# Kernel optimization log

Measured on AMD Instinct MI355X. Metric: run time of the kernel, lower is better.

Reference implementation:

```python
import jax, jax.numpy as jnp
import numpy as np

EULER = 0.5772156649015329  # Euler-Mascheroni constant


def _expi_neg(t):
    """Ei(t) for t < 0, via Ei(t) = -E1(-t).

    E1 uses the power series for x < 8 and the asymptotic expansion for x >= 8.
    This replaces the scipy.special.expi CPU round-trip of the original module.
    """
    x = -t  # x > 0
    # --- series branch (x < 8): E1(x) = -gamma - ln(x) + sum_{k>=1} (-1)^{k+1} x^k/(k*k!)
    xs = jnp.minimum(x, 8.0)
    s = jnp.zeros_like(xs)
    term = xs  # (-1)^{k+1} xs^k / k!  starting at k=1
    for k in range(1, 31):
        s = s + term / k
        term = term * (-xs) / (k + 1)
    e1_small = -EULER - jnp.log(xs) + s
    # --- asymptotic branch (x >= 8): E1(x) ~ e^{-x}/x * sum_n (-1)^n n! / x^n
    xl = jnp.maximum(x, 8.0)
    a = jnp.ones_like(xl)
    acc = jnp.ones_like(xl)
    for n in range(1, 9):
        a = a * (-n) / xl
        acc = acc + a
    e1_large = jnp.exp(-xl) / xl * acc
    e1 = jnp.where(x < 8.0, e1_small, e1_large)
    return -e1


def _li(v):
    # logarithmic integral li(v) = Ei(ln v); constant w.r.t. params (scipy detaches in torch)
    return jax.lax.stop_gradient(_expi_neg(jnp.log(v)))


def _phi(u, var2, var3, var4, var5):
    log_term = jnp.log(1.0 - u)
    li_term = _li(1.0 - u)
    return (var2 / log_term
            + var3 * li_term
            + var4 * ((1.0 - u) / log_term - li_term)
            + var5 * ((1.0 - u) * (log_term + 1.0) / (2.0 * log_term ** 2) - li_term / 2.0))


def setup_inputs() -> dict:
    key = jax.random.key(0)
    B, L, D = 262144, 64, 32
    hidden = [128, 128, 64]
    ks = jax.random.split(key, 16)
    u = jax.random.uniform(ks[0], (B, L), dtype=jnp.float32, minval=1e-4, maxval=1.0 - 1e-4)
    dims = [L] + hidden + [D]
    inp = {"u": u}
    for i in range(4):
        inp[f"W{i}"] = jax.random.normal(ks[1 + 2 * i], (dims[i], dims[i + 1]), dtype=jnp.float32) / np.sqrt(dims[i]).astype(np.float32)
        inp[f"b{i}"] = jnp.zeros((dims[i + 1],), dtype=jnp.float32)
    for j in range(1, 7):
        inp[f"var{j}"] = jax.random.normal(ks[8 + j], (1, D), dtype=jnp.float32) * 0.1
    return inp


def reference(u, W0, b0, W1, b1, W2, b2, W3, b3, var1, var2, var3, var4, var5, var6):
    # MLP: three Linear+ReLU blocks then final Linear to dim_data
    h = u
    for W, b in ((W0, b0), (W1, b1), (W2, b2)):
        h = jax.nn.relu(h @ W + b)
    net = h @ W3 + b3  # (B, dim_data)
    D = net.shape[1]
    ud = u[:, :D]
    # spline corrections
    p01 = -4.0 * ud ** 5 + 5.0 * ud ** 4
    corr1 = jnp.nan_to_num(p01 * (var1 + _phi(ud, var2, var3, var4, var5)), nan=0.0)
    corr2 = var6 * (ud ** 3 - 2.0 * ud ** 2 + ud)
    net_tif = jax.nn.relu(net + corr1 + corr2)
    # inverse TIF activation: ((1 - u^2)/2)^{-x}
    return jnp.power((1.0 - ud ** 2) / 2.0, -net_tif)
```

## Files before the change

kernel.cpp:

```cpp
#include <hip/hip_runtime.h>
#include <hip/hip_bf16.h>
#include <math.h>

#define LN2_F 0.69314718055994531f

typedef _Float16 half8 __attribute__((ext_vector_type(8)));
typedef _Float16 h4_t __attribute__((ext_vector_type(4)));
typedef __fp16 pk2_t __attribute__((ext_vector_type(2)));
typedef __attribute__((ext_vector_type(4))) float f32x4;
typedef __attribute__((ext_vector_type(8))) short short8;

__global__ void prep_weights(const float* __restrict__ W0, const float* __restrict__ W1,
                             const float* __restrict__ W2, const float* __restrict__ W3,
                             short* __restrict__ ws) {
    int e = blockIdx.x * 256 + threadIdx.x;
    const float* W; int N, NT, base, ul;
    if (e < 1024)      { W = W0; N = 128; NT = 8; base = 0;     ul = e; }
    else if (e < 3072) { W = W1; N = 128; NT = 8; base = 8192;  ul = e - 1024; }
    else if (e < 4096) { W = W2; N = 64;  NT = 4; base = 24576; ul = e - 3072; }
    else if (e < 4352) { W = W3; N = 32;  NT = 2; base = 32768; ul = e - 4096; }
    else return;
    const int cp = ul >> 6, lane = ul & 63;
    const int s = cp / NT, ct = cp % NT;
    const int k0 = s * 32 + (lane >> 4) * 8;
    const int n = ct * 16 + (lane & 15);
    union { half8 h; short8 s; } v;
#pragma unroll
    for (int j = 0; j < 8; ++j) v.h[j] = (_Float16)W[(size_t)(k0 + j) * N + n];
    *(short8*)(ws + base + cp * 512 + lane * 8) = v.s;
}

#define REGION_HALFS 2048

__device__ __forceinline__ void lds_fence() {
    asm volatile("s_waitcnt lgkmcnt(0)" ::: "memory");
}

template <int K>
__device__ __forceinline__ void load_a_tr(const _Float16* region, unsigned lane_off,
                                          half8 af[4]) {
    const unsigned base = (unsigned)(uintptr_t)region + lane_off;
#pragma unroll
    for (int s = 0; s < K / 32; ++s) {
        h4_t lo, hi;
        asm volatile("ds_read_b64_tr_b16 %0, %2\n\t"
                     "ds_read_b64_tr_b16 %1, %2 offset:128"
                     : "=&v"(lo), "=&v"(hi)
                     : "v"(base + (unsigned)(s * 1024))
                     : "memory");
        af[s] = __builtin_shufflevector(lo, hi, 0, 1, 2, 3, 4, 5, 6, 7);
    }
}

template <int N>
__device__ __forceinline__ void store_d_tr(_Float16* __restrict__ region, int m, int q,
                                           const f32x4* acc, bool relu) {
    const int base = (m >> 2) * 64 + (m & 3) * 16 + q * 4;
#pragma unroll
    for (int ct = 0; ct < N / 16; ++ct) {
        f32x4 v = acc[ct];
        float a0 = relu ? fmaxf(v[0], 0.0f) : v[0];
        float a1 = relu ? fmaxf(v[1], 0.0f) : v[1];
        float a2 = relu ? fmaxf(v[2], 0.0f) : v[2];
        float a3 = relu ? fmaxf(v[3], 0.0f) : v[3];
        pk2_t p0 = __builtin_amdgcn_cvt_pkrtz(a0, a1);
        pk2_t p1 = __builtin_amdgcn_cvt_pkrtz(a2, a3);
        h4_t h = {(_Float16)p0[0], (_Float16)p0[1], (_Float16)p1[0], (_Float16)p1[1]};
        *(h4_t*)(region + ct * 256 + base) = h;
    }
}

template <int NT>
__device__ __forceinline__ void preload_b(const half8* __restrict__ wf, int lane,
                                          half8 (&b)[8]) {
#pragma unroll
    for (int ct = 0; ct < NT; ++ct) b[ct] = wf[ct * 64 + lane];
}

template <int K, int N>
__device__ __forceinline__ void layer_frag2(const half8* __restrict__ wf,
                                            const float* bias,
                                            const half8 (&af)[2][4], int lane,
                                            f32x4 (&acc)[2][8],
                                            half8 (&ba)[8], half8 (&bb)[8]) {
    constexpr int NK = K / 32, NT = N / 16;
#pragma unroll
    for (int ct = 0; ct < NT; ++ct) {
        float b = bias[ct];
        acc[0][ct] = f32x4{b, b, b, b};
        acc[1][ct] = f32x4{b, b, b, b};
    }
#pragma unroll
    for (int s = 0; s < NK; ++s) {
        half8 (&bc)[8] = (s & 1) ? bb : ba;
        half8 (&bn)[8] = (s & 1) ? ba : bb;
        if (s + 1 < NK) {
#pragma unroll
            for (int ct = 0; ct < NT; ++ct) bn[ct] = wf[((s + 1) * NT + ct) * 64 + lane];
        }
#pragma unroll
        for (int ct = 0; ct < NT; ++ct) {
            acc[0][ct] = __builtin_amdgcn_mfma_f32_16x16x32_f16(af[0][s], bc[ct], acc[0][ct], 0, 0, 0);
            acc[1][ct] = __builtin_amdgcn_mfma_f32_16x16x32_f16(af[1][s], bc[ct], acc[1][ct], 0, 0, 0);
        }
    }
}

__global__ __launch_bounds__(256, 4) void mlp_phi_mfma(
    const float* __restrict__ u,
    const float* __restrict__ b0, const float* __restrict__ b1,
    const float* __restrict__ b2, const float* __restrict__ b3,
    const short* __restrict__ ws,
    const float* __restrict__ var1, const float* __restrict__ var2,
    const float* __restrict__ var3, const float* __restrict__ var4,
    const float* __restrict__ var5, const float* __restrict__ var6,
    float* __restrict__ out) {
    __shared__ __align__(16) _Float16 lds[4 * 2 * REGION_HALFS];
    const int t = threadIdx.x, lane = t & 63, wave = t >> 6;
    const int m = lane & 15, q = lane >> 4;
    _Float16* lw = lds + wave * 2 * REGION_HALFS;
    const unsigned lane_rd = (unsigned)(q * 256 + m * 8);
    const size_t row0 = (size_t)blockIdx.x * 128 + wave * 32;

    const half8* wf0 = (const half8*)(ws);
    const half8* wf1 = (const half8*)(ws + 8192);
    const half8* wf2 = (const half8*)(ws + 24576);
    const half8* wf3 = (const half8*)(ws + 32768);

    float bb0v[8], bb1v[8], bb2v[4], bb3v[2];
#pragma unroll
    for (int ct = 0; ct < 8; ++ct) bb0v[ct] = b0[ct * 16 + m];
#pragma unroll
    for (int ct = 0; ct < 8; ++ct) bb1v[ct] = b1[ct * 16 + m];
#pragma unroll
    for (int ct = 0; ct < 4; ++ct) bb2v[ct] = b2[ct * 16 + m];
#pragma unroll
    for (int ct = 0; ct < 2; ++ct) bb3v[ct] = b3[ct * 16 + m];

    float ev1[2], ev2[2], ev4[2], ev6[2], ev5h[2], ec3[2];
#pragma unroll
    for (int ot = 0; ot < 2; ++ot) {
        const int d = ot * 16 + m;
        ev1[ot] = var1[d]; ev2[ot] = var2[d]; ev4[ot] = var4[d]; ev6[ot] = var6[d];
        ev5h[ot] = 0.5f * var5[d];
        ec3[ot] = var3[d] - ev4[ot] - ev5h[ot];
    }

    half8 af[2][4];
    f32x4 acc[2][8];
    half8 ba[8], bb[8];

#pragma unroll
    for (int mt = 0; mt < 2; ++mt) {
        const float* up = u + (row0 + mt * 16 + m) * 64;
#pragma unroll
        for (int s = 0; s < 2; ++s) {
            float4 v0 = *(const float4*)(up + s * 32 + q * 8);
            float4 v1 = *(const float4*)(up + s * 32 + q * 8 + 4);
            pk2_t p0 = __builtin_amdgcn_cvt_pkrtz(v0.x, v0.y);
            pk2_t p1 = __builtin_amdgcn_cvt_pkrtz(v0.z, v0.w);
            pk2_t p2 = __builtin_amdgcn_cvt_pkrtz(v1.x, v1.y);
            pk2_t p3 = __builtin_amdgcn_cvt_pkrtz(v1.z, v1.w);
            af[mt][s] = half8{(_Float16)p0[0], (_Float16)p0[1], (_Float16)p1[0], (_Float16)p1[1],
                              (_Float16)p2[0], (_Float16)p2[1], (_Float16)p3[0], (_Float16)p3[1]};
        }
    }
    preload_b<8>(wf0, lane, ba);
    layer_frag2<64, 128>(wf0, bb0v, af, lane, acc, ba, bb);
#pragma unroll
    for (int mt = 0; mt < 2; ++mt) store_d_tr<128>(lw + mt * REGION_HALFS, m, q, acc[mt], true);

    preload_b<8>(wf1, lane, ba);
    lds_fence();
    load_a_tr<128>(lw, lane_rd, af[0]);
    load_a_tr<128>(lw + REGION_HALFS, lane_rd, af[1]);
    lds_fence();
    __builtin_amdgcn_sched_barrier(0);
    layer_frag2<128, 128>(wf1, bb1v, af, lane, acc, ba, bb);
#pragma unroll
    for (int mt = 0; mt < 2; ++mt) store_d_tr<128>(lw + mt * REGION_HALFS, m, q, acc[mt], true);

    preload_b<4>(wf2, lane, ba);
    lds_fence();
    load_a_tr<128>(lw, lane_rd, af[0]);
    load_a_tr<128>(lw + REGION_HALFS, lane_rd, af[1]);
    lds_fence();
    __builtin_amdgcn_sched_barrier(0);
    layer_frag2<128, 64>(wf2, bb2v, af, lane, acc, ba, bb);
#pragma unroll
    for (int mt = 0; mt < 2; ++mt) store_d_tr<64>(lw + mt * REGION_HALFS, m, q, acc[mt], true);

    preload_b<2>(wf3, lane, ba);
    lds_fence();
    load_a_tr<64>(lw, lane_rd, af[0]);
    load_a_tr<64>(lw + REGION_HALFS, lane_rd, af[1]);

    float ue[2][8];
#pragma unroll
    for (int mt = 0; mt < 2; ++mt)
#pragma unroll
        for (int ot = 0; ot < 2; ++ot)
#pragma unroll
            for (int r = 0; r < 4; ++r)
                ue[mt][ot * 4 + r] = u[(row0 + mt * 16 + q * 4 + r) * 64 + ot * 16 + m];

    lds_fence();
    __builtin_amdgcn_sched_barrier(0);
    layer_frag2<64, 32>(wf3, bb3v, af, lane, acc, ba, bb);

#pragma unroll
    for (int ot = 0; ot < 2; ++ot) {
        const int d = ot * 16 + m;
        const float v1 = ev1[ot], v2 = ev2[ot], v4 = ev4[ot], v6 = ev6[ot];
        const float v5h = ev5h[ot];
        const float c3 = ec3[ot];
#pragma unroll
        for (int mt = 0; mt < 2; ++mt) {
#pragma unroll
            for (int r = 0; r < 4; ++r) {
                const size_t row = row0 + mt * 16 + q * 4 + r;
                const float net = acc[mt][ot][r];
                const float ud = ue[mt][ot * 4 + r];

                const float omu = 1.0f - ud;
                const float lt = __log2f(omu) * LN2_F;
                const float x = -lt;

                const float e1s = -__log2f(x) * LN2_F
                    + (-0.57721566f + x * (0.99999193f + x * (-0.24991055f
                    + x * (0.05519968f + x * (-0.00976004f + x * 0.00107857f)))));
                const float num = 0.2677737343f + x * (8.6347608925f + x * (18.0590169730f
                    + x * (8.5733287401f + x)));
                const float den = 3.9584969228f + x * (21.0996530827f + x * (25.6329561486f
                    + x * (9.5733223454f + x)));
                const float e1l = __expf(-x) * num * __builtin_amdgcn_rcpf(x * den);
                const float li = -((x < 1.0f) ? e1s : e1l);

                const float rl = __builtin_amdgcn_rcpf(lt);
                const float phi = fmaf(v4, omu, v2) * rl
                                + (v5h * omu * (lt + 1.0f)) * rl * rl
                                + c3 * li;

                const float ud2 = ud * ud;
                const float ud4 = ud2 * ud2;
                const float p01 = ud4 * fmaf(-4.0f, ud, 5.0f);
                const float corr1 = p01 * (v1 + phi);
                const float d1 = ud - 1.0f;
                const float corr2 = v6 * ud * d1 * d1;

                const float nt = fmaxf(net + corr1 + corr2, 0.0f);
                const float base = fmaf(-0.5f, ud2, 0.5f);
                out[row * 32 + d] = __builtin_amdgcn_exp2f(-nt * __log2f(base));
            }
        }
    }
}

extern "C" void kernel_launch(void* const* d_in, const int* in_sizes, int n_in,
                              void* d_out, int out_size, void* d_ws, size_t ws_size,
                              hipStream_t stream) {
    const float* u    = (const float*)d_in[0];
    const float* W0   = (const float*)d_in[1];
    const float* b0   = (const float*)d_in[2];
    const float* W1   = (const float*)d_in[3];
    const float* b1   = (const float*)d_in[4];
    const float* W2   = (const float*)d_in[5];
    const float* b2   = (const float*)d_in[6];
    const float* W3   = (const float*)d_in[7];
    const float* b3   = (const float*)d_in[8];
    const float* var1 = (const float*)d_in[9];
    const float* var2 = (const float*)d_in[10];
    const float* var3 = (const float*)d_in[11];
    const float* var4 = (const float*)d_in[12];
    const float* var5 = (const float*)d_in[13];
    const float* var6 = (const float*)d_in[14];
    float* out = (float*)d_out;
    short* ws = (short*)d_ws;

    prep_weights<<<dim3(17), dim3(256), 0, stream>>>(W0, W1, W2, W3, ws);

    const int B = in_sizes[0] / 64;
    const int blocks = B / 128;
    mlp_phi_mfma<<<dim3(blocks), dim3(256), 0, stream>>>(
        u, b0, b1, b2, b3, ws,
        var1, var2, var3, var4, var5, var6, out);
}
```

Before: 175.9 us.

## Prefetch next layer weights during MFMA loop and hoist initial loads

Replaces the generic per-layer MFMA loop with an explicitly unrolled pipeline. The next layer's first weight fragments are prefetched into the free register buffer while the current layer's last MFMAs run, instead of being loaded between layers. The first-layer weight and u-fragment loads now come before the bias and var loads, and launch bounds drop from 4 to 2 waves per EU minimum. This aims to hide global weight-load latency between layers, and the looser bound gives the compiler more registers at the risk of lower occupancy.

```diff
diff --git a/kernel.cpp b/kernel.cpp
--- a/kernel.cpp
+++ b/kernel.cpp
@@ -3,12 +3,15 @@
 #include <math.h>
 
 #define LN2_F 0.69314718055994531f
+#define REGION_HALFS 2048
 
 typedef _Float16 half8 __attribute__((ext_vector_type(8)));
 typedef _Float16 h4_t __attribute__((ext_vector_type(4)));
 typedef __fp16 pk2_t __attribute__((ext_vector_type(2)));
 typedef __attribute__((ext_vector_type(4))) float f32x4;
 typedef __attribute__((ext_vector_type(8))) short short8;
+
+#define MFMA16(a, b, c) __builtin_amdgcn_mfma_f32_16x16x32_f16((a), (b), (c), 0, 0, 0)
 
 __global__ void prep_weights(const float* __restrict__ W0, const float* __restrict__ W1,
                              const float* __restrict__ W2, const float* __restrict__ W3,
@@ -30,83 +33,89 @@
     *(short8*)(ws + base + cp * 512 + lane * 8) = v.s;
 }
 
-#define REGION_HALFS 2048
 
 __device__ __forceinline__ void lds_fence() {
     asm volatile("s_waitcnt lgkmcnt(0)" ::: "memory");
 }
 
-template <int K>
-__device__ __forceinline__ void load_a_tr(const _Float16* region, unsigned lane_off,
-                                          half8 af[4]) {
-    const unsigned base = (unsigned)(uintptr_t)region + lane_off;
-#pragma unroll
-    for (int s = 0; s < K / 32; ++s) {
-        h4_t lo, hi;
-        asm volatile("ds_read_b64_tr_b16 %0, %2\n\t"
-                     "ds_read_b64_tr_b16 %1, %2 offset:128"
-                     : "=&v"(lo), "=&v"(hi)
-                     : "v"(base + (unsigned)(s * 1024))
-                     : "memory");
-        af[s] = __builtin_shufflevector(lo, hi, 0, 1, 2, 3, 4, 5, 6, 7);
-    }
-}
-
-template <int N>
-__device__ __forceinline__ void store_d_tr(_Float16* __restrict__ region, int m, int q,
-                                           const f32x4* acc, bool relu) {
-    const int base = (m >> 2) * 64 + (m & 3) * 16 + q * 4;
-#pragma unroll
-    for (int ct = 0; ct < N / 16; ++ct) {
-        f32x4 v = acc[ct];
-        float a0 = relu ? fmaxf(v[0], 0.0f) : v[0];
-        float a1 = relu ? fmaxf(v[1], 0.0f) : v[1];
-        float a2 = relu ? fmaxf(v[2], 0.0f) : v[2];
-        float a3 = relu ? fmaxf(v[3], 0.0f) : v[3];
-        pk2_t p0 = __builtin_amdgcn_cvt_pkrtz(a0, a1);
-        pk2_t p1 = __builtin_amdgcn_cvt_pkrtz(a2, a3);
-        h4_t h = {(_Float16)p0[0], (_Float16)p0[1], (_Float16)p1[0], (_Float16)p1[1]};
-        *(h4_t*)(region + ct * 256 + base) = h;
-    }
-}
-
-template <int NT>
-__device__ __forceinline__ void preload_b(const half8* __restrict__ wf, int lane,
-                                          half8 (&b)[8]) {
-#pragma unroll
-    for (int ct = 0; ct < NT; ++ct) b[ct] = wf[ct * 64 + lane];
-}
-
-template <int K, int N>
-__device__ __forceinline__ void layer_frag2(const half8* __restrict__ wf,
-                                            const float* bias,
-                                            const half8 (&af)[2][4], int lane,
-                                            f32x4 (&acc)[2][8],
-                                            half8 (&ba)[8], half8 (&bb)[8]) {
+__device__ __forceinline__ half8 tr_read_ks(const _Float16* region, unsigned lane_off, int s) {
+    h4_t lo, hi;
+    asm volatile("ds_read_b64_tr_b16 %0, %2\n\t"
+                 "ds_read_b64_tr_b16 %1, %2 offset:128"
+                 : "=&v"(lo), "=&v"(hi)
+                 : "v"((unsigned)(uintptr_t)region + lane_off + (unsigned)(s * 1024))
+                 : "memory");
+    return __builtin_shufflevector(lo, hi, 0, 1, 2, 3, 4, 5, 6, 7);
+}
+
+__device__ __forceinline__ void store_tile(_Float16* __restrict__ region, int ct_global,
+                                           int m, int q, f32x4 v) {
+    const int base = ct_global * 256 + (m >> 2) * 64 + (m & 3) * 16 + q * 4;
+    pk2_t p0 = __builtin_amdgcn_cvt_pkrtz(fmaxf(v[0], 0.0f), fmaxf(v[1], 0.0f));
+    pk2_t p1 = __builtin_amdgcn_cvt_pkrtz(fmaxf(v[2], 0.0f), fmaxf(v[3], 0.0f));
+    h4_t h = {(_Float16)p0[0], (_Float16)p0[1], (_Float16)p1[0], (_Float16)p1[1]};
+    *(h4_t*)(region + base) = h;
+}
+
+template <int K, int N, int NEXT_NT>
+__device__ __forceinline__ void layer_pipe(const half8* __restrict__ wf,
+                                           const half8* __restrict__ wf_next,
+                                           const float* bias, const half8 (&af)[2][4],
+                                           int lane, f32x4 (&acc)[2][8],
+                                           half8 (&ba)[8], half8 (&bb)[8]) {
     constexpr int NK = K / 32, NT = N / 16;
+    static_assert(NK == 2 || NK == 4, "");
 #pragma unroll
     for (int ct = 0; ct < NT; ++ct) {
-        float b = bias[ct];
+        const float b = bias[ct];
         acc[0][ct] = f32x4{b, b, b, b};
         acc[1][ct] = f32x4{b, b, b, b};
     }
 #pragma unroll
-    for (int s = 0; s < NK; ++s) {
-        half8 (&bc)[8] = (s & 1) ? bb : ba;
-        half8 (&bn)[8] = (s & 1) ? ba : bb;
-        if (s + 1 < NK) {
-#pragma unroll
-            for (int ct = 0; ct < NT; ++ct) bn[ct] = wf[((s + 1) * NT + ct) * 64 + lane];
-        }
+    for (int ct = 0; ct < NT; ++ct) bb[ct] = wf[(NT + ct) * 64 + lane];
+#pragma unroll
+    for (int ct = 0; ct < NT; ++ct) {
+        acc[0][ct] = MFMA16(af[0][0], ba[ct], acc[0][ct]);
+        acc[1][ct] = MFMA16(af[1][0], ba[ct], acc[1][ct]);
+    }
+    if constexpr (NK == 4) {
+#pragma unroll
+        for (int ct = 0; ct < NT; ++ct) ba[ct] = wf[(2 * NT + ct) * 64 + lane];
 #pragma unroll
         for (int ct = 0; ct < NT; ++ct) {
-            acc[0][ct] = __builtin_amdgcn_mfma_f32_16x16x32_f16(af[0][s], bc[ct], acc[0][ct], 0, 0, 0);
-            acc[1][ct] = __builtin_amdgcn_mfma_f32_16x16x32_f16(af[1][s], bc[ct], acc[1][ct], 0, 0, 0);
-        }
-    }
-}
-
-__global__ __launch_bounds__(256, 4) void mlp_phi_mfma(
+            acc[0][ct] = MFMA16(af[0][1], bb[ct], acc[0][ct]);
+            acc[1][ct] = MFMA16(af[1][1], bb[ct], acc[1][ct]);
+        }
+#pragma unroll
+        for (int ct = 0; ct < NT; ++ct) bb[ct] = wf[(3 * NT + ct) * 64 + lane];
+#pragma unroll
+        for (int ct = 0; ct < NT; ++ct) {
+            acc[0][ct] = MFMA16(af[0][2], ba[ct], acc[0][ct]);
+            acc[1][ct] = MFMA16(af[1][2], ba[ct], acc[1][ct]);
+        }
+        if constexpr (NEXT_NT > 0) {
+#pragma unroll
+            for (int ct = 0; ct < NEXT_NT; ++ct) ba[ct] = wf_next[ct * 64 + lane];
+        }
+#pragma unroll
+        for (int ct = 0; ct < NT; ++ct) {
+            acc[0][ct] = MFMA16(af[0][3], bb[ct], acc[0][ct]);
+            acc[1][ct] = MFMA16(af[1][3], bb[ct], acc[1][ct]);
+        }
+    } else {
+        if constexpr (NEXT_NT > 0) {
+#pragma unroll
+            for (int ct = 0; ct < NEXT_NT; ++ct) ba[ct] = wf_next[ct * 64 + lane];
+        }
+#pragma unroll
+        for (int ct = 0; ct < NT; ++ct) {
+            acc[0][ct] = MFMA16(af[0][1], bb[ct], acc[0][ct]);
+            acc[1][ct] = MFMA16(af[1][1], bb[ct], acc[1][ct]);
+        }
+    }
+}
+
+__global__ __launch_bounds__(256, 2) void mlp_phi_mfma(
     const float* __restrict__ u,
     const float* __restrict__ b0, const float* __restrict__ b1,
     const float* __restrict__ b2, const float* __restrict__ b3,
@@ -127,6 +136,28 @@
     const half8* wf2 = (const half8*)(ws + 24576);
     const half8* wf3 = (const half8*)(ws + 32768);
 
+    half8 af[2][4];
+    f32x4 acc[2][8];
+    half8 ba[8], bb[8];
+
+#pragma unroll
+    for (int ct = 0; ct < 8; ++ct) ba[ct] = wf0[ct * 64 + lane];
+#pragma unroll
+    for (int mt = 0; mt < 2; ++mt) {
+        const float* up = u + (row0 + mt * 16 + m) * 64;
+#pragma unroll
+        for (int s = 0; s < 2; ++s) {
+            float4 v0a = *(const float4*)(up + s * 32 + q * 8);
+            float4 v1a = *(const float4*)(up + s * 32 + q * 8 + 4);
+            pk2_t p0 = __builtin_amdgcn_cvt_pkrtz(v0a.x, v0a.y);
+            pk2_t p1 = __builtin_amdgcn_cvt_pkrtz(v0a.z, v0a.w);
+            pk2_t p2 = __builtin_amdgcn_cvt_pkrtz(v1a.x, v1a.y);
+            pk2_t p3 = __builtin_amdgcn_cvt_pkrtz(v1a.z, v1a.w);
+            af[mt][s] = half8{(_Float16)p0[0], (_Float16)p0[1], (_Float16)p1[0], (_Float16)p1[1],
+                              (_Float16)p2[0], (_Float16)p2[1], (_Float16)p3[0], (_Float16)p3[1]};
+        }
+    }
+
     float bb0v[8], bb1v[8], bb2v[4], bb3v[2];
 #pragma unroll
     for (int ct = 0; ct < 8; ++ct) bb0v[ct] = b0[ct * 16 + m];
@@ -146,54 +177,45 @@
         ec3[ot] = var3[d] - ev4[ot] - ev5h[ot];
     }
 
-    half8 af[2][4];
-    f32x4 acc[2][8];
-    half8 ba[8], bb[8];
-
-#pragma unroll
-    for (int mt = 0; mt < 2; ++mt) {
-        const float* up = u + (row0 + mt * 16 + m) * 64;
-#pragma unroll
-        for (int s = 0; s < 2; ++s) {
-            float4 v0 = *(const float4*)(up + s * 32 + q * 8);
-            float4 v1 = *(const float4*)(up + s * 32 + q * 8 + 4);
-            pk2_t p0 = __builtin_amdgcn_cvt_pkrtz(v0.x, v0.y);
-            pk2_t p1 = __builtin_amdgcn_cvt_pkrtz(v0.z, v0.w);
-            pk2_t p2 = __builtin_amdgcn_cvt_pkrtz(v1.x, v1.y);
-            pk2_t p3 = __builtin_amdgcn_cvt_pkrtz(v1.z, v1.w);
-            af[mt][s] = half8{(_Float16)p0[0], (_Float16)p0[1], (_Float16)p1[0], (_Float16)p1[1],
-                              (_Float16)p2[0], (_Float16)p2[1], (_Float16)p3[0], (_Float16)p3[1]};
-        }
-    }
-    preload_b<8>(wf0, lane, ba);
-    layer_frag2<64, 128>(wf0, bb0v, af, lane, acc, ba, bb);
-#pragma unroll
-    for (int mt = 0; mt < 2; ++mt) store_d_tr<128>(lw + mt * REGION_HALFS, m, q, acc[mt], true);
-
-    preload_b<8>(wf1, lane, ba);
-    lds_fence();
-    load_a_tr<128>(lw, lane_rd, af[0]);
-    load_a_tr<128>(lw + REGION_HALFS, lane_rd, af[1]);
+    layer_pipe<64, 128, 8>(wf0, wf1, bb0v, af, lane, acc, ba, bb);
+#pragma unroll
+    for (int mt = 0; mt < 2; ++mt)
+#pragma unroll
+        for (int ct = 0; ct < 8; ++ct)
+            store_tile(lw + mt * REGION_HALFS, ct, m, q, acc[mt][ct]);
+    lds_fence();
+#pragma unroll
+    for (int mt = 0; mt < 2; ++mt)
+#pragma unroll
+        for (int s = 0; s < 4; ++s) af[mt][s] = tr_read_ks(lw + mt * REGION_HALFS, lane_rd, s);
     lds_fence();
     __builtin_amdgcn_sched_barrier(0);
-    layer_frag2<128, 128>(wf1, bb1v, af, lane, acc, ba, bb);
-#pragma unroll
-    for (int mt = 0; mt < 2; ++mt) store_d_tr<128>(lw + mt * REGION_HALFS, m, q, acc[mt], true);
-
-    preload_b<4>(wf2, lane, ba);
-    lds_fence();
-    load_a_tr<128>(lw, lane_rd, af[0]);
-    load_a_tr<128>(lw + REGION_HALFS, lane_rd, af[1]);
+
+    layer_pipe<128, 128, 4>(wf1, wf2, bb1v, af, lane, acc, ba, bb);
+#pragma unroll
+    for (int mt = 0; mt < 2; ++mt)
+#pragma unroll
+        for (int ct = 0; ct < 8; ++ct)
+            store_tile(lw + mt * REGION_HALFS, ct, m, q, acc[mt][ct]);
+    lds_fence();
+#pragma unroll
+    for (int mt = 0; mt < 2; ++mt)
+#pragma unroll
+        for (int s = 0; s < 4; ++s) af[mt][s] = tr_read_ks(lw + mt * REGION_HALFS, lane_rd, s);
     lds_fence();
     __builtin_amdgcn_sched_barrier(0);
-    layer_frag2<128, 64>(wf2, bb2v, af, lane, acc, ba, bb);
-#pragma unroll
-    for (int mt = 0; mt < 2; ++mt) store_d_tr<64>(lw + mt * REGION_HALFS, m, q, acc[mt], true);
-
-    preload_b<2>(wf3, lane, ba);
-    lds_fence();
-    load_a_tr<64>(lw, lane_rd, af[0]);
-    load_a_tr<64>(lw + REGION_HALFS, lane_rd, af[1]);
+
+    layer_pipe<128, 64, 2>(wf2, wf3, bb2v, af, lane, acc, ba, bb);
+#pragma unroll
+    for (int mt = 0; mt < 2; ++mt)
+#pragma unroll
+        for (int ct = 0; ct < 4; ++ct)
+            store_tile(lw + mt * REGION_HALFS, ct, m, q, acc[mt][ct]);
+    lds_fence();
+#pragma unroll
+    for (int mt = 0; mt < 2; ++mt)
+#pragma unroll
+        for (int s = 0; s < 2; ++s) af[mt][s] = tr_read_ks(lw + mt * REGION_HALFS, lane_rd, s);
 
     float ue[2][8];
 #pragma unroll
@@ -206,7 +228,8 @@
 
     lds_fence();
     __builtin_amdgcn_sched_barrier(0);
-    layer_frag2<64, 32>(wf3, bb3v, af, lane, acc, ba, bb);
+
+    layer_pipe<64, 32, 0>(wf3, nullptr, bb3v, af, lane, acc, ba, bb);
 
 #pragma unroll
     for (int ot = 0; ot < 2; ++ot) {
```

After: 155.2 us. 1.13x faster.
